# Performance work log

Measured on AMD Instinct MI355X. Metric: run time of the kernel, lower is better.

Reference implementation:

```python
import jax, jax.numpy as jnp
import numpy as np

B, F_IN, F_OUT, D, K = 32, 64, 64, 512, 64


def setup_inputs() -> dict:
    key = jax.random.key(0)
    k1, k2, k3 = jax.random.split(key, 3)
    x = jax.random.normal(k1, (B, F_IN, D), dtype=jnp.float32)
    # Evaluated monomial-word operators: K matrices of size D x D
    word_ops = jax.random.normal(k2, (K, D, D), dtype=jnp.float32)
    # nn.init.uniform_ -> U[0,1)
    coeff = jax.random.uniform(k3, (F_OUT, F_IN, K), dtype=jnp.float32)
    return {"x": x, "word_ops": word_ops, "coeff": coeff}


def reference(x, word_ops, coeff):
    # Per sample in the torch code:
    #   evals[i, d, k] = (X @ W_k)[i, d] = sum_e X[i, e] * W[k, e, d]
    #   res = tensordot(coeff, evals, ([1, 2], [0, 2]))  -> [F_out, D]
    # Fully batched fused contraction (replaces the Python loop over batch):
    # evals: [B, F_in, D, K]
    evals = jnp.einsum('bie,ked->bidk', x, word_ops)
    # out: [B, F_out, D]
    out = jnp.einsum('oik,bidk->bod', coeff, evals)
    return out
```

## Files before the change

### kernel.cpp

```cpp
#include <hip/hip_runtime.h>


#define KK 32768

typedef __attribute__((ext_vector_type(8))) short bf16x8;
typedef __attribute__((ext_vector_type(4))) float f32x4;

__device__ __forceinline__ unsigned short f2bf(float f) {
  unsigned int u = __float_as_uint(f);
  return (unsigned short)((u + 0x7FFFu + ((u >> 16) & 1u)) >> 16);
}

__device__ __forceinline__ void gld16(void* lds, const void* g) {
  __builtin_amdgcn_global_load_lds((const __attribute__((address_space(1))) void*)g,
                                   (__attribute__((address_space(3))) void*)lds,
                                   16, 0, 0);
}

__global__ __launch_bounds__(256) void convW(const float* __restrict__ W,
                                             unsigned short* __restrict__ WbT) {
  __shared__ float tile[64][65];
  int bx = blockIdx.x;
  int k = bx >> 6, et = (bx >> 3) & 7, dt = bx & 7;
  int t = threadIdx.x;
  const float* src = W + ((size_t)k * 512 + (size_t)et * 64) * 512 + dt * 64;
  int rr = t >> 6, cc = t & 63;
#pragma unroll
  for (int p = 0; p < 16; p++) {
    int e = p * 4 + rr;
    tile[e][cc] = src[(size_t)e * 512 + cc];
  }
  __syncthreads();
  int dl = t >> 4, eg = t & 15;
#pragma unroll
  for (int p = 0; p < 4; p++) {
    int d = p * 16 + dl;
    ushort4 v;
    v.x = f2bf(tile[eg * 4 + 0][d]);
    v.y = f2bf(tile[eg * 4 + 1][d]);
    v.z = f2bf(tile[eg * 4 + 2][d]);
    v.w = f2bf(tile[eg * 4 + 3][d]);
    *(ushort4*)(WbT + (size_t)(dt * 64 + d) * KK + k * 512 + et * 64 + eg * 4) = v;
  }
}

__global__ __launch_bounds__(256) void convXC(const float* __restrict__ x,
                                              const float* __restrict__ c,
                                              unsigned short* __restrict__ xT,
                                              unsigned short* __restrict__ cb) {
  __shared__ unsigned short lds[64 * 130];
  int t = threadIdx.x;
  if (blockIdx.x < 128) {
    int bx = blockIdx.x;
    int b = bx >> 2, ec = bx & 3;
    const float* src = x + (size_t)b * 32768 + ec * 128;
#pragma unroll
    for (int j = 0; j < 32; j++) {
      int idx = j * 256 + t;
      int i = idx >> 7, e = idx & 127;
      lds[i * 130 + e] = f2bf(src[(size_t)i * 512 + e]);
    }
    __syncthreads();
    unsigned short* dst = xT + (size_t)b * 32768 + ec * 128 * 64;
#pragma unroll
    for (int j = 0; j < 32; j++) {
      int idx = j * 256 + t;
      int e = idx >> 6, i = idx & 63;
      dst[idx] = lds[i * 130 + e];
    }
  } else {
    int rb = blockIdx.x - 128;
    const float* src = c + (size_t)rb * 4096;
#pragma unroll
    for (int j = 0; j < 16; j++) {
      int idx = j * 256 + t;
      int r = idx >> 6, k = idx & 63;
      lds[r * 66 + k] = f2bf(src[idx]);
    }
    __syncthreads();
#pragma unroll
    for (int j = 0; j < 16; j++) {
      int idx = j * 256 + t;
      int k = idx >> 6, r = idx & 63;
      cb[(size_t)k * 4096 + rb * 64 + r] = lds[r * 66 + k];
    }
  }
}

__global__ __launch_bounds__(256, 3) void fused_kern(const unsigned short* __restrict__ xT,
                                                     const unsigned short* __restrict__ cb,
                                                     const unsigned short* __restrict__ Bt,
                                                     float* __restrict__ out) {
  __shared__ unsigned short u[128 * 64];
  __shared__ unsigned short Bs[128 * 64];
  __shared__ unsigned short ck[2][64 * 64];
  int bx = blockIdx.x;
  int ks = bx & 15, nt = (bx >> 4) & 3, mt = bx >> 6;
  int m0 = mt * 128, n0 = nt * 128, kw0 = ks * 4, b0 = mt * 2;
  int t = threadIdx.x;
  int wid = t >> 6, lane = t & 63, q = lane >> 4, l16 = lane & 15;
  int wmb = wid & 1;
  int weh = wid >> 1;
  int srow = t >> 3;
  int cg = (t & 7) ^ (srow & 7);
  {
    const unsigned short* gc = cb + (size_t)kw0 * 4096;
#pragma unroll
    for (int j = 0; j < 2; j++)
      gld16((char*)ck[0] + (j * 256 + t) * 16, gc + (j * 32 + srow) * 64 + cg * 8);
  }
  f32x4 acc[4][4] = {};
#pragma unroll 1
  for (int ec = 0; ec < 8; ec++) {
#pragma unroll
    for (int j = 0; j < 4; j++) {
      int row = j * 32 + srow;
      int bl = row >> 6, el = row & 63;
      gld16((char*)u + (j * 256 + t) * 16,
            xT + (size_t)(b0 + bl) * 32768 + (size_t)(ec * 64 + el) * 64 + cg * 8);
    }
    __syncthreads();
    bf16x8 ax[2][2];
#pragma unroll
    for (int ef = 0; ef < 2; ef++)
#pragma unroll
      for (int ks2 = 0; ks2 < 2; ks2++) {
        int row = wmb * 64 + weh * 32 + ef * 16 + l16;
        int s2 = (ks2 * 4 + q) ^ (row & 7);
        ax[ef][ks2] = *(const bf16x8*)(u + row * 64 + s2 * 8);
      }
    __syncthreads();
#pragma unroll 1
    for (int k = 0; k < 4; k++) {
      int seq = ec * 4 + k, cur = seq & 1;
      const unsigned short* gb = Bt + (size_t)n0 * KK + (size_t)(kw0 + k) * 512 + ec * 64;
#pragma unroll
      for (int j = 0; j < 4; j++) {
        int row = j * 32 + srow;
        gld16((char*)Bs + (j * 256 + t) * 16, gb + (size_t)row * KK + cg * 8);
      }
      if (seq < 31) {
        int nk = (k < 3) ? k + 1 : 0;
        const unsigned short* gc = cb + (size_t)(kw0 + nk) * 4096;
#pragma unroll
        for (int j = 0; j < 2; j++)
          gld16((char*)ck[cur ^ 1] + (j * 256 + t) * 16, gc + (j * 32 + srow) * 64 + cg * 8);
      }
      const unsigned short* ckk = ck[cur];
      bf16x8 bc[4][2];
#pragma unroll
      for (int of = 0; of < 4; of++)
#pragma unroll
        for (int ks2 = 0; ks2 < 2; ks2++) {
          int o = of * 16 + l16;
          int s2 = (ks2 * 4 + q) ^ (o & 7);
          bc[of][ks2] = *(const bf16x8*)(ckk + o * 64 + s2 * 8);
        }
      f32x4 td[2][4] = {};
#pragma unroll
      for (int ef = 0; ef < 2; ef++)
#pragma unroll
        for (int of = 0; of < 4; of++)
#pragma unroll
          for (int ks2 = 0; ks2 < 2; ks2++)
            td[ef][of] = __builtin_amdgcn_mfma_f32_16x16x32_bf16(ax[ef][ks2], bc[of][ks2],
                                                                 td[ef][of], 0, 0, 0);
#pragma unroll
      for (int ef = 0; ef < 2; ef++)
#pragma unroll
        for (int of = 0; of < 4; of++) {
          int row = wmb * 64 + of * 16 + l16;
          int c0 = weh * 32 + ef * 16 + q * 4;
          int phys = ((c0 >> 3) ^ (row & 7)) * 8 + (c0 & 7);
          ushort4 v;
          v.x = f2bf(td[ef][of][0]);
          v.y = f2bf(td[ef][of][1]);
          v.z = f2bf(td[ef][of][2]);
          v.w = f2bf(td[ef][of][3]);
          *(ushort4*)(u + row * 64 + phys) = v;
        }
      __syncthreads();
#pragma unroll
      for (int ks2 = 0; ks2 < 2; ks2++) {
        int slot = ks2 * 4 + q;
        bf16x8 af[4], bfr[4];
#pragma unroll
        for (int fr = 0; fr < 4; fr++) {
          int row = wmb * 64 + fr * 16 + l16;
          af[fr] = *(const bf16x8*)(u + row * 64 + (slot ^ (row & 7)) * 8);
        }
#pragma unroll
        for (int fc = 0; fc < 4; fc++) {
          int row = weh * 64 + fc * 16 + l16;
          bfr[fc] = *(const bf16x8*)(Bs + row * 64 + (slot ^ (row & 7)) * 8);
        }
#pragma unroll
        for (int fr = 0; fr < 4; fr++)
#pragma unroll
          for (int fc = 0; fc < 4; fc++)
            acc[fr][fc] = __builtin_amdgcn_mfma_f32_16x16x32_bf16(af[fr], bfr[fc],
                                                                  acc[fr][fc], 0, 0, 0);
      }
      __syncthreads();
    }
  }
#pragma unroll
  for (int fr = 0; fr < 4; fr++)
#pragma unroll
    for (int fc = 0; fc < 4; fc++)
#pragma unroll
      for (int r = 0; r < 4; r++)
        atomicAdd(&out[(size_t)(m0 + wmb * 64 + fr * 16 + q * 4 + r) * 512
                       + n0 + weh * 64 + fc * 16 + l16],
                  acc[fr][fc][r]);
}

__global__ __launch_bounds__(256) void fallback_kern(const float* __restrict__ x,
                                                     const float* __restrict__ W,
                                                     const float* __restrict__ coeff,
                                                     float* __restrict__ out) {
  __shared__ float ev[64][129];
  int b = blockIdx.x >> 6, k = blockIdx.x & 63;
  int t = threadIdx.x, dl = t & 127, half = t >> 7;
  const float* xb = x + (size_t)b * 64 * 512;
  const float* Wk = W + (size_t)k * 512 * 512;
  for (int dc = 0; dc < 4; dc++) {
    int d = dc * 128 + dl;
    for (int i = half * 32; i < half * 32 + 32; i++) {
      float acc = 0.f;
      const float* xr = xb + (size_t)i * 512;
#pragma unroll 4
      for (int e = 0; e < 512; e++) acc += xr[e] * Wk[(size_t)e * 512 + d];
      ev[i][dl] = acc;
    }
    __syncthreads();
    for (int o = half * 32; o < half * 32 + 32; o++) {
      float s = 0.f;
#pragma unroll 8
      for (int i = 0; i < 64; i++) s += coeff[((size_t)o * 64 + i) * 64 + k] * ev[i][dl];
      atomicAdd(&out[((size_t)(b * 64 + o)) * 512 + d], s);
    }
    __syncthreads();
  }
}

extern "C" void kernel_launch(void* const* d_in, const int* in_sizes, int n_in,
                              void* d_out, int out_size, void* d_ws, size_t ws_size,
                              hipStream_t stream) {
  const float* x = (const float*)d_in[0];
  const float* W = (const float*)d_in[1];
  const float* coeff = (const float*)d_in[2];
  float* out = (float*)d_out;
  const size_t OFF_XT = 33554432;
  const size_t OFF_CB = OFF_XT + 2097152;
  const size_t NEED = OFF_CB + 524288;

  hipMemsetAsync(d_out, 0, (size_t)out_size * sizeof(float), stream);
  if (ws_size >= NEED) {
    unsigned short* WbT = (unsigned short*)d_ws;
    unsigned short* xT  = (unsigned short*)((char*)d_ws + OFF_XT);
    unsigned short* cb  = (unsigned short*)((char*)d_ws + OFF_CB);
    convXC<<<192, 256, 0, stream>>>(x, coeff, xT, cb);
    convW<<<4096, 256, 0, stream>>>(W, WbT);
    fused_kern<<<1024, 256, 0, stream>>>(xT, cb, WbT, out);
  } else {
    fallback_kern<<<2048, 256, 0, stream>>>(x, W, coeff, out);
  }
}
```

Measured before the change: 229.0 us.

## Widen fused kernel N tile to 256 and preload all coeff slices

Doubles each block's output tile along D from 128 to 256 columns, halving the grid to 512 blocks. Each block now recomputes the x·coeff intermediate half as often relative to the W traffic, and the warp layout is reworked so each wave computes all four e-fragments for two o-fragments. All four coefficient slices are loaded into LDS once up front instead of double-buffered per step, and bf16 packing uses the paired intrinsic. The cost is more accumulator registers, occupancy dropping from 3 to 2 blocks per CU, and fewer blocks to fill the GPU.

```diff
diff --git a/kernel.cpp b/kernel.cpp
--- a/kernel.cpp
+++ b/kernel.cpp
@@ -1,4 +1,5 @@
 #include <hip/hip_runtime.h>
+#include <hip/hip_bf16.h>
 
 
 #define KK 32768
@@ -9,6 +10,11 @@
 __device__ __forceinline__ unsigned short f2bf(float f) {
   unsigned int u = __float_as_uint(f);
   return (unsigned short)((u + 0x7FFFu + ((u >> 16) & 1u)) >> 16);
+}
+
+__device__ __forceinline__ unsigned int pkbf2(float a, float b) {
+  __hip_bfloat162 h = __float22bfloat162_rn(make_float2(a, b));
+  return *(unsigned int*)&h;
 }
 
 __device__ __forceinline__ void gld16(void* lds, const void* g) {
@@ -87,29 +93,31 @@
   }
 }
 
-__global__ __launch_bounds__(256, 3) void fused_kern(const unsigned short* __restrict__ xT,
+__global__ __launch_bounds__(256, 2) void fused_kern(const unsigned short* __restrict__ xT,
                                                      const unsigned short* __restrict__ cb,
                                                      const unsigned short* __restrict__ Bt,
                                                      float* __restrict__ out) {
   __shared__ unsigned short u[128 * 64];
-  __shared__ unsigned short Bs[128 * 64];
-  __shared__ unsigned short ck[2][64 * 64];
+  __shared__ unsigned short Bs[256 * 64];
+  __shared__ unsigned short ck[4 * 64 * 64];
   int bx = blockIdx.x;
-  int ks = bx & 15, nt = (bx >> 4) & 3, mt = bx >> 6;
-  int m0 = mt * 128, n0 = nt * 128, kw0 = ks * 4, b0 = mt * 2;
+  int ks = bx & 15, np = (bx >> 4) & 1, mt = bx >> 5;
+  int m0 = mt * 128, n0 = np * 256, kw0 = ks * 4, b0 = mt * 2;
   int t = threadIdx.x;
   int wid = t >> 6, lane = t & 63, q = lane >> 4, l16 = lane & 15;
   int wmb = wid & 1;
-  int weh = wid >> 1;
+  int wnh = wid >> 1;
   int srow = t >> 3;
   int cg = (t & 7) ^ (srow & 7);
   {
     const unsigned short* gc = cb + (size_t)kw0 * 4096;
 #pragma unroll
-    for (int j = 0; j < 2; j++)
-      gld16((char*)ck[0] + (j * 256 + t) * 16, gc + (j * 32 + srow) * 64 + cg * 8);
-  }
-  f32x4 acc[4][4] = {};
+    for (int j = 0; j < 8; j++) {
+      int row = j * 32 + srow;
+      gld16((char*)ck + (j * 256 + t) * 16, gc + (size_t)row * 64 + cg * 8);
+    }
+  }
+  f32x4 acc[4][8] = {};
 #pragma unroll 1
   for (int ec = 0; ec < 8; ec++) {
 #pragma unroll
@@ -120,99 +128,88 @@
             xT + (size_t)(b0 + bl) * 32768 + (size_t)(ec * 64 + el) * 64 + cg * 8);
     }
     __syncthreads();
-    bf16x8 ax[2][2];
-#pragma unroll
-    for (int ef = 0; ef < 2; ef++)
+    bf16x8 ax[4][2];
+#pragma unroll
+    for (int et = 0; et < 4; et++)
 #pragma unroll
       for (int ks2 = 0; ks2 < 2; ks2++) {
-        int row = wmb * 64 + weh * 32 + ef * 16 + l16;
+        int row = wmb * 64 + et * 16 + l16;
         int s2 = (ks2 * 4 + q) ^ (row & 7);
-        ax[ef][ks2] = *(const bf16x8*)(u + row * 64 + s2 * 8);
+        ax[et][ks2] = *(const bf16x8*)(u + row * 64 + s2 * 8);
       }
     __syncthreads();
 #pragma unroll 1
     for (int k = 0; k < 4; k++) {
-      int seq = ec * 4 + k, cur = seq & 1;
       const unsigned short* gb = Bt + (size_t)n0 * KK + (size_t)(kw0 + k) * 512 + ec * 64;
 #pragma unroll
-      for (int j = 0; j < 4; j++) {
+      for (int j = 0; j < 8; j++) {
         int row = j * 32 + srow;
         gld16((char*)Bs + (j * 256 + t) * 16, gb + (size_t)row * KK + cg * 8);
       }
-      if (seq < 31) {
-        int nk = (k < 3) ? k + 1 : 0;
-        const unsigned short* gc = cb + (size_t)(kw0 + nk) * 4096;
-#pragma unroll
-        for (int j = 0; j < 2; j++)
-          gld16((char*)ck[cur ^ 1] + (j * 256 + t) * 16, gc + (j * 32 + srow) * 64 + cg * 8);
-      }
-      const unsigned short* ckk = ck[cur];
-      bf16x8 bc[4][2];
-#pragma unroll
-      for (int of = 0; of < 4; of++)
+      const unsigned short* ckk = ck + k * 4096;
+      bf16x8 bc[2][2];
+#pragma unroll
+      for (int otl = 0; otl < 2; otl++)
 #pragma unroll
         for (int ks2 = 0; ks2 < 2; ks2++) {
-          int o = of * 16 + l16;
+          int o = (wnh * 2 + otl) * 16 + l16;
           int s2 = (ks2 * 4 + q) ^ (o & 7);
-          bc[of][ks2] = *(const bf16x8*)(ckk + o * 64 + s2 * 8);
-        }
-      f32x4 td[2][4] = {};
-#pragma unroll
-      for (int ef = 0; ef < 2; ef++)
-#pragma unroll
-        for (int of = 0; of < 4; of++)
+          bc[otl][ks2] = *(const bf16x8*)(ckk + o * 64 + s2 * 8);
+        }
+      f32x4 td[4][2] = {};
+#pragma unroll
+      for (int et = 0; et < 4; et++)
+#pragma unroll
+        for (int otl = 0; otl < 2; otl++)
 #pragma unroll
           for (int ks2 = 0; ks2 < 2; ks2++)
-            td[ef][of] = __builtin_amdgcn_mfma_f32_16x16x32_bf16(ax[ef][ks2], bc[of][ks2],
-                                                                 td[ef][of], 0, 0, 0);
-#pragma unroll
-      for (int ef = 0; ef < 2; ef++)
-#pragma unroll
-        for (int of = 0; of < 4; of++) {
-          int row = wmb * 64 + of * 16 + l16;
-          int c0 = weh * 32 + ef * 16 + q * 4;
+            td[et][otl] = __builtin_amdgcn_mfma_f32_16x16x32_bf16(ax[et][ks2], bc[otl][ks2],
+                                                                  td[et][otl], 0, 0, 0);
+#pragma unroll
+      for (int et = 0; et < 4; et++)
+#pragma unroll
+        for (int otl = 0; otl < 2; otl++) {
+          int row = wmb * 64 + (wnh * 2 + otl) * 16 + l16;
+          int c0 = et * 16 + q * 4;
           int phys = ((c0 >> 3) ^ (row & 7)) * 8 + (c0 & 7);
-          ushort4 v;
-          v.x = f2bf(td[ef][of][0]);
-          v.y = f2bf(td[ef][of][1]);
-          v.z = f2bf(td[ef][of][2]);
-          v.w = f2bf(td[ef][of][3]);
-          *(ushort4*)(u + row * 64 + phys) = v;
+          uint2 v;
+          v.x = pkbf2(td[et][otl][0], td[et][otl][1]);
+          v.y = pkbf2(td[et][otl][2], td[et][otl][3]);
+          *(uint2*)(u + row * 64 + phys) = v;
         }
       __syncthreads();
 #pragma unroll
       for (int ks2 = 0; ks2 < 2; ks2++) {
-        int slot = ks2 * 4 + q;
-        bf16x8 af[4], bfr[4];
-#pragma unroll
-        for (int fr = 0; fr < 4; fr++) {
-          int row = wmb * 64 + fr * 16 + l16;
-          af[fr] = *(const bf16x8*)(u + row * 64 + (slot ^ (row & 7)) * 8);
-        }
-#pragma unroll
-        for (int fc = 0; fc < 4; fc++) {
-          int row = weh * 64 + fc * 16 + l16;
-          bfr[fc] = *(const bf16x8*)(Bs + row * 64 + (slot ^ (row & 7)) * 8);
-        }
-#pragma unroll
-        for (int fr = 0; fr < 4; fr++)
-#pragma unroll
-          for (int fc = 0; fc < 4; fc++)
-            acc[fr][fc] = __builtin_amdgcn_mfma_f32_16x16x32_bf16(af[fr], bfr[fc],
-                                                                  acc[fr][fc], 0, 0, 0);
+        bf16x8 af[4], bfr[8];
+#pragma unroll
+        for (int mf = 0; mf < 4; mf++) {
+          int row = wmb * 64 + mf * 16 + l16;
+          af[mf] = *(const bf16x8*)(u + row * 64 + (((ks2 * 4 + q) ^ (row & 7))) * 8);
+        }
+#pragma unroll
+        for (int nf = 0; nf < 8; nf++) {
+          int row = wnh * 128 + nf * 16 + l16;
+          bfr[nf] = *(const bf16x8*)(Bs + row * 64 + (((ks2 * 4 + q) ^ (row & 7))) * 8);
+        }
+#pragma unroll
+        for (int mf = 0; mf < 4; mf++)
+#pragma unroll
+          for (int nf = 0; nf < 8; nf++)
+            acc[mf][nf] = __builtin_amdgcn_mfma_f32_16x16x32_bf16(af[mf], bfr[nf],
+                                                                  acc[mf][nf], 0, 0, 0);
       }
       __syncthreads();
     }
   }
 #pragma unroll
-  for (int fr = 0; fr < 4; fr++)
-#pragma unroll
-    for (int fc = 0; fc < 4; fc++)
+  for (int mf = 0; mf < 4; mf++)
+#pragma unroll
+    for (int nf = 0; nf < 8; nf++)
 #pragma unroll
       for (int r = 0; r < 4; r++)
-        atomicAdd(&out[(size_t)(m0 + wmb * 64 + fr * 16 + q * 4 + r) * 512
-                       + n0 + weh * 64 + fc * 16 + l16],
-                  acc[fr][fc][r]);
+        atomicAdd(&out[(size_t)(m0 + wmb * 64 + mf * 16 + q * 4 + r) * 512
+                       + n0 + wnh * 128 + nf * 16 + l16],
+                  acc[mf][nf][r]);
 }
 
 __global__ __launch_bounds__(256) void fallback_kern(const float* __restrict__ x,
@@ -262,7 +259,7 @@
     unsigned short* cb  = (unsigned short*)((char*)d_ws + OFF_CB);
     convXC<<<192, 256, 0, stream>>>(x, coeff, xT, cb);
     convW<<<4096, 256, 0, stream>>>(W, WbT);
-    fused_kern<<<1024, 256, 0, stream>>>(xT, cb, WbT, out);
+    fused_kern<<<512, 256, 0, stream>>>(xT, cb, WbT, out);
   } else {
     fallback_kern<<<2048, 256, 0, stream>>>(x, W, coeff, out);
   }
```

Result: faster. 221.9 us (-3.1%).
